# Optimization experiments

Hardware: AMD Instinct MI355X
Metric: run time of the kernel (lower is better)

## Reference

```python
import jax, jax.numpy as jnp
import numpy as np

NEG_INF = -4294967295.0  # -2**32 + 1, matches original padding value

def prelu(x, alpha):
    return jnp.where(x >= 0, x, alpha * x)

def setup_inputs() -> dict:
    key = jax.random.key(0)
    ks = jax.random.split(key, 12)
    B, T, D = 2048, 200, 64
    H0, H1 = 80, 40
    q = jax.random.normal(ks[0], (B, D), dtype=jnp.float32)
    k = jax.random.normal(ks[1], (B, T, D), dtype=jnp.float32)
    v = jax.random.normal(ks[2], (B, T, D), dtype=jnp.float32)
    mask = jax.random.randint(ks[3], (B, T), 0, 2, dtype=jnp.int32)
    Fin = 4 * D  # concat of q, k, q-k, q*k
    W0 = jax.random.normal(ks[4], (Fin, H0), dtype=jnp.float32) / np.sqrt(Fin)
    b0 = jnp.zeros((H0,), dtype=jnp.float32)
    a0 = jax.random.uniform(ks[5], (H0,), dtype=jnp.float32) * 0.25  # PReLU per-feature alpha
    W1 = jax.random.normal(ks[6], (H0, H1), dtype=jnp.float32) / np.sqrt(H0)
    b1 = jnp.zeros((H1,), dtype=jnp.float32)
    a1 = jax.random.uniform(ks[7], (H1,), dtype=jnp.float32) * 0.25
    Wo = jax.random.normal(ks[8], (H1, 1), dtype=jnp.float32) / np.sqrt(H1)
    bo = jnp.zeros((1,), dtype=jnp.float32)
    return {"q": q, "k": k, "v": v, "W0": W0, "b0": b0, "a0": a0,
            "W1": W1, "b1": b1, "a1": a1, "Wo": Wo, "bo": bo, "mask": mask}

def reference(q, k, v, W0, b0, a0, W1, b1, a1, Wo, bo, mask):
    # q: [B,D] -> broadcast to [B,T,D] (tile+reshape in original)
    qe = jnp.broadcast_to(q[:, None, :], k.shape)
    info = jnp.concatenate([qe, k, qe - k, qe * k], axis=-1)  # [B,T,4D]
    h = prelu(jnp.einsum('btf,fh->bth', info, W0) + b0, a0)    # [B,T,H0]
    h = prelu(jnp.einsum('bth,hg->btg', h, W1) + b1, a1)       # [B,T,H1]
    logits = (jnp.einsum('btg,go->bto', h, Wo) + bo)[..., 0]   # [B,T]
    logits = jnp.where(mask == 0, NEG_INF, logits)
    w = jax.nn.softmax(logits, axis=-1)                        # [B,T]
    out = jnp.einsum('bt,btd->bd', w, v)                       # [B,D]
    return out
```

## Files before the change

### kernel.cpp

```cpp
#include <hip/hip_runtime.h>
#include <hip/hip_bf16.h>
#include <math.h>

constexpr int D  = 64;
constexpr int T  = 200;
constexpr int H0 = 80;
constexpr int H1 = 40;
constexpr int BLOCK = 256;
constexpr float NEG_INF_V = -4294967295.0f;

typedef short short8 __attribute__((ext_vector_type(8)));
typedef float f32x4 __attribute__((ext_vector_type(4)));
typedef int   int4v __attribute__((ext_vector_type(4)));

__device__ inline unsigned short bf16h(float x) {
    __hip_bfloat16 t = __float2bfloat16(x);
    union { __hip_bfloat16 v; unsigned short u; } c; c.v = t; return c.u;
}
__device__ inline unsigned pk_bf16(float a, float b) {
    float2 f2; f2.x = a; f2.y = b;
    __hip_bfloat162 t = __float22bfloat162_rn(f2);
    union { __hip_bfloat162 v; unsigned u; } c; c.v = t; return c.u;
}
__device__ inline void pk_split(float a, float b, unsigned& hi, unsigned& lo) {
    hi = pk_bf16(a, b);
    const float e0 = a - __uint_as_float(hi << 16);
    const float e1 = b - __uint_as_float(hi & 0xffff0000u);
    lo = pk_bf16(e0, e1);
}
__device__ inline short8 mk8(int w0, int w1, int w2, int w3) {
    union { int4v i; short8 s; } u;
    u.i = (int4v){w0, w1, w2, w3};
    return u.s;
}
#define BPERM(ad, v) __builtin_amdgcn_ds_bpermute((ad), (int)(v))
#define MFMA(A, B, C) __builtin_amdgcn_mfma_f32_16x16x32_bf16((A), (B), (C), 0, 0, 0)

__global__ __launch_bounds__(BLOCK, 2) void attn_fused(
    const float* __restrict__ q, const float* __restrict__ k,
    const float* __restrict__ v, const float* __restrict__ W0,
    const float* __restrict__ b0, const float* __restrict__ a0,
    const float* __restrict__ W1, const float* __restrict__ b1,
    const float* __restrict__ a1, const float* __restrict__ Wo,
    const int* __restrict__ mask, float* __restrict__ out)
{
    __shared__ unsigned short s_wfHi[5120];
    __shared__ unsigned short s_wfLo[5120];
    __shared__ unsigned short s_w1Hi[4608];
    __shared__ unsigned short s_w1Lo[4608];
    __shared__ float s_logits[208];
    __shared__ float s_biasq[H0];
    __shared__ float s_a0[H0];
    __shared__ float s_b1p[48], s_a1p[48], s_Wop[48];
    __shared__ float s_w[BLOCK];
    __shared__ float s_red[8];
    __shared__ float s_part[4][D];

    const int tid  = threadIdx.x;
    const int b    = blockIdx.x;
    const int wv   = tid >> 6;
    const int lane = tid & 63;
    const int l16  = lane & 15;
    const int quad = lane >> 4;
    const bool hiQ = (quad >= 2);
    const float* qb = q + (size_t)b * D;

    const int mval = (tid < T) ? mask[(size_t)b * T + tid] : 0;
    float4 kc0, kc1, kc2, kc3;
    {
        int row = wv * 16 + l16; if (row > T - 1) row = T - 1;
        const float* kr = k + ((size_t)b * T + row) * D + quad * 8;
        kc0 = *(const float4*)(kr);
        kc1 = *(const float4*)(kr + 4);
        kc2 = *(const float4*)(kr + 32);
        kc3 = *(const float4*)(kr + 36);
    }

    const float* Wk = W0 + 64 * H0;
    const float* Wd = W0 + 128 * H0;
    const float* Wp = W0 + 192 * H0;
    #pragma unroll 4
    for (int it = 0; it < 20; ++it) {
        const int e  = it * 256 + tid;
        const int kk = e / 80, h = e - kk * 80;
        const float w = Wk[e] - Wd[e] + qb[kk] * Wp[e];
        const unsigned short hb = bf16h(w);
        const unsigned short lb = bf16h(w - __uint_as_float((unsigned)hb << 16));
        const int off = (((kk >> 5) * 5 + (h >> 4)) << 9)
                      + (((((kk >> 3) & 3) << 4) + (h & 15)) << 3) + (kk & 7);
        s_wfHi[off] = hb; s_wfLo[off] = lb;
    }
    #pragma unroll 4
    for (int it = 0; it < 18; ++it) {
        const int e  = it * 256 + tid;
        const int k2 = e / 48, n = e - k2 * 48;
        const float w = (k2 < H0 && n < H1) ? W1[k2 * H1 + n] : 0.0f;
        const unsigned short hb = bf16h(w);
        const unsigned short lb = bf16h(w - __uint_as_float((unsigned)hb << 16));
        const int off = (((k2 >> 5) * 3 + (n >> 4)) << 9)
                      + (((((k2 >> 3) & 3) << 4) + (n & 15)) << 3) + (k2 & 7);
        s_w1Hi[off] = hb; s_w1Lo[off] = lb;
    }
    if (tid < H0) {
        float acc = b0[tid];
        #pragma unroll 8
        for (int d = 0; d < D; ++d)
            acc = fmaf(qb[d], W0[d * H0 + tid] + W0[(128 + d) * H0 + tid], acc);
        s_biasq[tid] = acc;
        s_a0[tid]    = a0[tid];
    }
    if (tid < 48) {
        s_b1p[tid] = (tid < H1) ? b1[tid] : 0.0f;
        s_a1p[tid] = (tid < H1) ? a1[tid] : 0.0f;
        s_Wop[tid] = (tid < H1) ? Wo[tid] : 0.0f;
    }
    __syncthreads();

    const int addr0 = (((quad & 1) << 5) + l16) << 2;
    const int addr1 = addr0 + 64;

#define L1_HT(HT, HW, LW) { \
    f32x4 acc_ = {0.0f, 0.0f, 0.0f, 0.0f}; \
    { short8 Ah_ = *(const short8*)&s_wfHi[(0 * 5 + HT) * 512 + lane * 8]; \
      short8 Al_ = *(const short8*)&s_wfLo[(0 * 5 + HT) * 512 + lane * 8]; \
      acc_ = MFMA(Ah_, kbhi0, acc_); \
      acc_ = MFMA(Ah_, kblo0, acc_); \
      acc_ = MFMA(Al_, kbhi0, acc_); } \
    { short8 Ah_ = *(const short8*)&s_wfHi[(1 * 5 + HT) * 512 + lane * 8]; \
      short8 Al_ = *(const short8*)&s_wfLo[(1 * 5 + HT) * 512 + lane * 8]; \
      acc_ = MFMA(Ah_, kbhi1, acc_); \
      acc_ = MFMA(Ah_, kblo1, acc_); \
      acc_ = MFMA(Al_, kbhi1, acc_); } \
    const int hb_ = HT * 16 + quad * 4; \
    const float x0_ = acc_[0] + s_biasq[hb_ + 0]; \
    const float x1_ = acc_[1] + s_biasq[hb_ + 1]; \
    const float x2_ = acc_[2] + s_biasq[hb_ + 2]; \
    const float x3_ = acc_[3] + s_biasq[hb_ + 3]; \
    const float f0_ = (x0_ >= 0.0f) ? x0_ : s_a0[hb_ + 0] * x0_; \
    const float f1_ = (x1_ >= 0.0f) ? x1_ : s_a0[hb_ + 1] * x1_; \
    const float f2_ = (x2_ >= 0.0f) ? x2_ : s_a0[hb_ + 2] * x2_; \
    const float f3_ = (x3_ >= 0.0f) ? x3_ : s_a0[hb_ + 3] * x3_; \
    pk_split(f0_, f1_, HW.x, LW.x); \
    pk_split(f2_, f3_, HW.y, LW.y); }

#define TRN(HA, HB, LA, LB, AHI, ALO) { \
    int h0_ = BPERM(addr0, HA.x), h1_ = BPERM(addr0, HA.y); \
    int h2_ = BPERM(addr1, HA.x), h3_ = BPERM(addr1, HA.y); \
    int g0_ = BPERM(addr0, HB.x), g1_ = BPERM(addr0, HB.y); \
    int g2_ = BPERM(addr1, HB.x), g3_ = BPERM(addr1, HB.y); \
    AHI = mk8(hiQ ? g0_ : h0_, hiQ ? g1_ : h1_, hiQ ? g2_ : h2_, hiQ ? g3_ : h3_); \
    int l0_ = BPERM(addr0, LA.x), l1_ = BPERM(addr0, LA.y); \
    int l2_ = BPERM(addr1, LA.x), l3_ = BPERM(addr1, LA.y); \
    int m0_ = BPERM(addr0, LB.x), m1_ = BPERM(addr0, LB.y); \
    int m2_ = BPERM(addr1, LB.x), m3_ = BPERM(addr1, LB.y); \
    ALO = mk8(hiQ ? m0_ : l0_, hiQ ? m1_ : l1_, hiQ ? m2_ : l2_, hiQ ? m3_ : l3_); }

#define TRN2(HA, LA, AHI, ALO) { \
    int h0_ = BPERM(addr0, HA.x), h1_ = BPERM(addr0, HA.y); \
    int h2_ = BPERM(addr1, HA.x), h3_ = BPERM(addr1, HA.y); \
    AHI = mk8(hiQ ? 0 : h0_, hiQ ? 0 : h1_, hiQ ? 0 : h2_, hiQ ? 0 : h3_); \
    int l0_ = BPERM(addr0, LA.x), l1_ = BPERM(addr0, LA.y); \
    int l2_ = BPERM(addr1, LA.x), l3_ = BPERM(addr1, LA.y); \
    ALO = mk8(hiQ ? 0 : l0_, hiQ ? 0 : l1_, hiQ ? 0 : l2_, hiQ ? 0 : l3_); }

#define L2_NT(NT2) { \
    f32x4 acc_ = {0.0f, 0.0f, 0.0f, 0.0f}; \
    { short8 bh_ = *(const short8*)&s_w1Hi[(0 * 3 + NT2) * 512 + lane * 8]; \
      short8 bl_ = *(const short8*)&s_w1Lo[(0 * 3 + NT2) * 512 + lane * 8]; \
      acc_ = MFMA(a2hi0, bh_, acc_); \
      acc_ = MFMA(a2hi0, bl_, acc_); \
      acc_ = MFMA(a2lo0, bh_, acc_); } \
    { short8 bh_ = *(const short8*)&s_w1Hi[(1 * 3 + NT2) * 512 + lane * 8]; \
      short8 bl_ = *(const short8*)&s_w1Lo[(1 * 3 + NT2) * 512 + lane * 8]; \
      acc_ = MFMA(a2hi1, bh_, acc_); \
      acc_ = MFMA(a2hi1, bl_, acc_); \
      acc_ = MFMA(a2lo1, bh_, acc_); } \
    { short8 bh_ = *(const short8*)&s_w1Hi[(2 * 3 + NT2) * 512 + lane * 8]; \
      short8 bl_ = *(const short8*)&s_w1Lo[(2 * 3 + NT2) * 512 + lane * 8]; \
      acc_ = MFMA(a2hi2, bh_, acc_); \
      acc_ = MFMA(a2hi2, bl_, acc_); \
      acc_ = MFMA(a2lo2, bh_, acc_); } \
    const int g_ = NT2 * 16 + l16; \
    const float bg_ = s_b1p[g_], ag_ = s_a1p[g_], wg_ = s_Wop[g_]; \
    { const float x_ = acc_[0] + bg_; part0 = fmaf((x_ >= 0.0f) ? x_ : ag_ * x_, wg_, part0); } \
    { const float x_ = acc_[1] + bg_; part1 = fmaf((x_ >= 0.0f) ? x_ : ag_ * x_, wg_, part1); } \
    { const float x_ = acc_[2] + bg_; part2 = fmaf((x_ >= 0.0f) ? x_ : ag_ * x_, wg_, part2); } \
    { const float x_ = acc_[3] + bg_; part3 = fmaf((x_ >= 0.0f) ? x_ : ag_ * x_, wg_, part3); } }

    for (int mt = wv; mt < 13; mt += 4) {
        float4 kn0, kn1, kn2, kn3;
        const bool hasNext = (mt + 4 < 13);
        if (hasNext) {
            int row = (mt + 4) * 16 + l16; if (row > T - 1) row = T - 1;
            const float* kr = k + ((size_t)b * T + row) * D + quad * 8;
            kn0 = *(const float4*)(kr);
            kn1 = *(const float4*)(kr + 4);
            kn2 = *(const float4*)(kr + 32);
            kn3 = *(const float4*)(kr + 36);
        }
        short8 kbhi0, kblo0, kbhi1, kblo1;
        {
            unsigned h0_, l0_, h1_, l1_, h2_, l2_, h3_, l3_;
            pk_split(kc0.x, kc0.y, h0_, l0_);
            pk_split(kc0.z, kc0.w, h1_, l1_);
            pk_split(kc1.x, kc1.y, h2_, l2_);
            pk_split(kc1.z, kc1.w, h3_, l3_);
            kbhi0 = mk8((int)h0_, (int)h1_, (int)h2_, (int)h3_);
            kblo0 = mk8((int)l0_, (int)l1_, (int)l2_, (int)l3_);
            pk_split(kc2.x, kc2.y, h0_, l0_);
            pk_split(kc2.z, kc2.w, h1_, l1_);
            pk_split(kc3.x, kc3.y, h2_, l2_);
            pk_split(kc3.z, kc3.w, h3_, l3_);
            kbhi1 = mk8((int)h0_, (int)h1_, (int)h2_, (int)h3_);
            kblo1 = mk8((int)l0_, (int)l1_, (int)l2_, (int)l3_);
        }
        uint2 hw0, hw1, hw2, hw3, hw4, lw0, lw1, lw2, lw3, lw4;
        L1_HT(0, hw0, lw0)
        L1_HT(1, hw1, lw1)
        L1_HT(2, hw2, lw2)
        L1_HT(3, hw3, lw3)
        L1_HT(4, hw4, lw4)
        short8 a2hi0, a2lo0, a2hi1, a2lo1, a2hi2, a2lo2;
        TRN(hw0, hw1, lw0, lw1, a2hi0, a2lo0)
        TRN(hw2, hw3, lw2, lw3, a2hi1, a2lo1)
        TRN2(hw4, lw4, a2hi2, a2lo2)
        float part0 = 0.0f, part1 = 0.0f, part2 = 0.0f, part3 = 0.0f;
        L2_NT(0)
        L2_NT(1)
        L2_NT(2)
        #pragma unroll
        for (int off = 1; off < 16; off <<= 1) {
            part0 += __shfl_xor(part0, off);
            part1 += __shfl_xor(part1, off);
            part2 += __shfl_xor(part2, off);
            part3 += __shfl_xor(part3, off);
        }
        if (l16 == 0) {
            float4 p = {part0, part1, part2, part3};
            *(float4*)&s_logits[mt * 16 + quad * 4] = p;
        }
        if (hasNext) { kc0 = kn0; kc1 = kn1; kc2 = kn2; kc3 = kn3; }
    }
    __syncthreads();

    float logit = -INFINITY;
    if (tid < T)
        logit = (mval == 0) ? NEG_INF_V : s_logits[tid];

    float m = logit;
    #pragma unroll
    for (int off = 32; off > 0; off >>= 1) m = fmaxf(m, __shfl_xor(m, off));
    if (lane == 0) s_red[wv] = m;
    __syncthreads();
    m = fmaxf(fmaxf(s_red[0], s_red[1]), fmaxf(s_red[2], s_red[3]));
    const float e = expf(logit - m);
    s_w[tid] = e;
    float ssum = e;
    #pragma unroll
    for (int off = 32; off > 0; off >>= 1) ssum += __shfl_xor(ssum, off);
    if (lane == 0) s_red[4 + wv] = ssum;
    __syncthreads();
    const float inv = 1.0f / (s_red[4] + s_red[5] + s_red[6] + s_red[7]);

    const int d = tid & (D - 1);
    const int c = tid >> 6;
    constexpr int TC = T / 4;
    float acc2 = 0.0f;
    const float* vp = v + ((size_t)b * T + c * TC) * D + d;
    #pragma unroll 10
    for (int t = 0; t < TC; ++t)
        acc2 = fmaf(s_w[c * TC + t], vp[t * D], acc2);
    s_part[c][d] = acc2;
    __syncthreads();
    if (tid < D) {
        out[(size_t)b * D + tid] =
            (s_part[0][tid] + s_part[1][tid] + s_part[2][tid] + s_part[3][tid]) * inv;
    }
}

extern "C" void kernel_launch(void* const* d_in, const int* in_sizes, int n_in,
                              void* d_out, int out_size, void* d_ws, size_t ws_size,
                              hipStream_t stream) {
    const float* q  = (const float*)d_in[0];
    const float* k  = (const float*)d_in[1];
    const float* v  = (const float*)d_in[2];
    const float* W0 = (const float*)d_in[3];
    const float* b0 = (const float*)d_in[4];
    const float* a0 = (const float*)d_in[5];
    const float* W1 = (const float*)d_in[6];
    const float* b1 = (const float*)d_in[7];
    const float* a1 = (const float*)d_in[8];
    const float* Wo = (const float*)d_in[9];
    const int*  mask = (const int*)d_in[11];
    float* out = (float*)d_out;

    const int B = in_sizes[0] / D;

    attn_fused<<<dim3(B), dim3(BLOCK), 0, stream>>>(
        q, k, v, W0, b0, a0, W1, b1, a1, Wo, mask, out);
}
```

Baseline: 323.4 us.

## Process two row tiles per wave iteration with interleaved MFMA chains

Each wave now handles two 16-row k tiles at once (A and B), running their MFMA accumulation chains interleaved so independent MFMAs can hide each other's latency. Shared-memory weight fragments are loaded once and reused for both tiles, and the prefetch of k rows is doubled accordingly. The 13-tile loop becomes two iterations, with some tiles clamped to tile 12 and computed redundantly. The cost is higher register pressure and redundant work on the clamped tiles.

```diff
diff --git a/kernel.cpp b/kernel.cpp
--- a/kernel.cpp
+++ b/kernel.cpp
@@ -64,16 +64,19 @@
     const int quad = lane >> 4;
     const bool hiQ = (quad >= 2);
     const float* qb = q + (size_t)b * D;
+    const float* kb_base = k + (size_t)b * T * D;
 
     const int mval = (tid < T) ? mask[(size_t)b * T + tid] : 0;
-    float4 kc0, kc1, kc2, kc3;
+    float4 kA0, kA1, kA2, kA3, kB0, kB1, kB2, kB3;
     {
-        int row = wv * 16 + l16; if (row > T - 1) row = T - 1;
-        const float* kr = k + ((size_t)b * T + row) * D + quad * 8;
-        kc0 = *(const float4*)(kr);
-        kc1 = *(const float4*)(kr + 4);
-        kc2 = *(const float4*)(kr + 32);
-        kc3 = *(const float4*)(kr + 36);
+        int rA = wv * 16 + l16;        if (rA > T - 1) rA = T - 1;
+        int rB = (wv + 4) * 16 + l16;  if (rB > T - 1) rB = T - 1;
+        const float* pA = kb_base + (size_t)rA * D + quad * 8;
+        const float* pB = kb_base + (size_t)rB * D + quad * 8;
+        kA0 = *(const float4*)(pA);      kB0 = *(const float4*)(pB);
+        kA1 = *(const float4*)(pA + 4);  kB1 = *(const float4*)(pB + 4);
+        kA2 = *(const float4*)(pA + 32); kB2 = *(const float4*)(pB + 32);
+        kA3 = *(const float4*)(pA + 36); kB3 = *(const float4*)(pB + 36);
     }
 
     const float* Wk = W0 + 64 * H0;
@@ -119,29 +122,48 @@
     const int addr0 = (((quad & 1) << 5) + l16) << 2;
     const int addr1 = addr0 + 64;
 
-#define L1_HT(HT, HW, LW) { \
-    f32x4 acc_ = {0.0f, 0.0f, 0.0f, 0.0f}; \
-    { short8 Ah_ = *(const short8*)&s_wfHi[(0 * 5 + HT) * 512 + lane * 8]; \
-      short8 Al_ = *(const short8*)&s_wfLo[(0 * 5 + HT) * 512 + lane * 8]; \
-      acc_ = MFMA(Ah_, kbhi0, acc_); \
-      acc_ = MFMA(Ah_, kblo0, acc_); \
-      acc_ = MFMA(Al_, kbhi0, acc_); } \
-    { short8 Ah_ = *(const short8*)&s_wfHi[(1 * 5 + HT) * 512 + lane * 8]; \
-      short8 Al_ = *(const short8*)&s_wfLo[(1 * 5 + HT) * 512 + lane * 8]; \
-      acc_ = MFMA(Ah_, kbhi1, acc_); \
-      acc_ = MFMA(Ah_, kblo1, acc_); \
-      acc_ = MFMA(Al_, kbhi1, acc_); } \
+#define KBUILD(C0, C1, C2, C3, BH0, BL0, BH1, BL1) { \
+    unsigned h0_, l0_, h1_, l1_, h2_, l2_, h3_, l3_; \
+    pk_split(C0.x, C0.y, h0_, l0_); pk_split(C0.z, C0.w, h1_, l1_); \
+    pk_split(C1.x, C1.y, h2_, l2_); pk_split(C1.z, C1.w, h3_, l3_); \
+    BH0 = mk8((int)h0_, (int)h1_, (int)h2_, (int)h3_); \
+    BL0 = mk8((int)l0_, (int)l1_, (int)l2_, (int)l3_); \
+    pk_split(C2.x, C2.y, h0_, l0_); pk_split(C2.z, C2.w, h1_, l1_); \
+    pk_split(C3.x, C3.y, h2_, l2_); pk_split(C3.z, C3.w, h3_, l3_); \
+    BH1 = mk8((int)h0_, (int)h1_, (int)h2_, (int)h3_); \
+    BL1 = mk8((int)l0_, (int)l1_, (int)l2_, (int)l3_); }
+
+#define L1_NT(HT, HWA, LWA, HWB, LWB) { \
+    const short8 Ah0_ = *(const short8*)&s_wfHi[(0 * 5 + HT) * 512 + lane * 8]; \
+    const short8 Al0_ = *(const short8*)&s_wfLo[(0 * 5 + HT) * 512 + lane * 8]; \
+    const short8 Ah1_ = *(const short8*)&s_wfHi[(1 * 5 + HT) * 512 + lane * 8]; \
+    const short8 Al1_ = *(const short8*)&s_wfLo[(1 * 5 + HT) * 512 + lane * 8]; \
+    f32x4 aA_ = {0.0f, 0.0f, 0.0f, 0.0f}, aB_ = {0.0f, 0.0f, 0.0f, 0.0f}; \
+    aA_ = MFMA(Ah0_, kAhi0, aA_);  aB_ = MFMA(Ah0_, kBhi0, aB_); \
+    aA_ = MFMA(Ah0_, kAlo0, aA_);  aB_ = MFMA(Ah0_, kBlo0, aB_); \
+    aA_ = MFMA(Al0_, kAhi0, aA_);  aB_ = MFMA(Al0_, kBhi0, aB_); \
+    aA_ = MFMA(Ah1_, kAhi1, aA_);  aB_ = MFMA(Ah1_, kBhi1, aB_); \
+    aA_ = MFMA(Ah1_, kAlo1, aA_);  aB_ = MFMA(Ah1_, kBlo1, aB_); \
+    aA_ = MFMA(Al1_, kAhi1, aA_);  aB_ = MFMA(Al1_, kBhi1, aB_); \
     const int hb_ = HT * 16 + quad * 4; \
-    const float x0_ = acc_[0] + s_biasq[hb_ + 0]; \
-    const float x1_ = acc_[1] + s_biasq[hb_ + 1]; \
-    const float x2_ = acc_[2] + s_biasq[hb_ + 2]; \
-    const float x3_ = acc_[3] + s_biasq[hb_ + 3]; \
-    const float f0_ = (x0_ >= 0.0f) ? x0_ : s_a0[hb_ + 0] * x0_; \
-    const float f1_ = (x1_ >= 0.0f) ? x1_ : s_a0[hb_ + 1] * x1_; \
-    const float f2_ = (x2_ >= 0.0f) ? x2_ : s_a0[hb_ + 2] * x2_; \
-    const float f3_ = (x3_ >= 0.0f) ? x3_ : s_a0[hb_ + 3] * x3_; \
-    pk_split(f0_, f1_, HW.x, LW.x); \
-    pk_split(f2_, f3_, HW.y, LW.y); }
+    const float c0_ = s_biasq[hb_ + 0], c1_ = s_biasq[hb_ + 1]; \
+    const float c2_ = s_biasq[hb_ + 2], c3_ = s_biasq[hb_ + 3]; \
+    const float p0_ = s_a0[hb_ + 0], p1_ = s_a0[hb_ + 1]; \
+    const float p2_ = s_a0[hb_ + 2], p3_ = s_a0[hb_ + 3]; \
+    { const float x0_ = aA_[0] + c0_, x1_ = aA_[1] + c1_; \
+      const float x2_ = aA_[2] + c2_, x3_ = aA_[3] + c3_; \
+      const float f0_ = (x0_ >= 0.0f) ? x0_ : p0_ * x0_; \
+      const float f1_ = (x1_ >= 0.0f) ? x1_ : p1_ * x1_; \
+      const float f2_ = (x2_ >= 0.0f) ? x2_ : p2_ * x2_; \
+      const float f3_ = (x3_ >= 0.0f) ? x3_ : p3_ * x3_; \
+      pk_split(f0_, f1_, HWA.x, LWA.x); pk_split(f2_, f3_, HWA.y, LWA.y); } \
+    { const float x0_ = aB_[0] + c0_, x1_ = aB_[1] + c1_; \
+      const float x2_ = aB_[2] + c2_, x3_ = aB_[3] + c3_; \
+      const float f0_ = (x0_ >= 0.0f) ? x0_ : p0_ * x0_; \
+      const float f1_ = (x1_ >= 0.0f) ? x1_ : p1_ * x1_; \
+      const float f2_ = (x2_ >= 0.0f) ? x2_ : p2_ * x2_; \
+      const float f3_ = (x3_ >= 0.0f) ? x3_ : p3_ * x3_; \
+      pk_split(f0_, f1_, HWB.x, LWB.x); pk_split(f2_, f3_, HWB.y, LWB.y); } }
 
 #define TRN(HA, HB, LA, LB, AHI, ALO) { \
     int h0_ = BPERM(addr0, HA.x), h1_ = BPERM(addr0, HA.y); \
@@ -164,82 +186,92 @@
     ALO = mk8(hiQ ? 0 : l0_, hiQ ? 0 : l1_, hiQ ? 0 : l2_, hiQ ? 0 : l3_); }
 
 #define L2_NT(NT2) { \
-    f32x4 acc_ = {0.0f, 0.0f, 0.0f, 0.0f}; \
-    { short8 bh_ = *(const short8*)&s_w1Hi[(0 * 3 + NT2) * 512 + lane * 8]; \
-      short8 bl_ = *(const short8*)&s_w1Lo[(0 * 3 + NT2) * 512 + lane * 8]; \
-      acc_ = MFMA(a2hi0, bh_, acc_); \
-      acc_ = MFMA(a2hi0, bl_, acc_); \
-      acc_ = MFMA(a2lo0, bh_, acc_); } \
-    { short8 bh_ = *(const short8*)&s_w1Hi[(1 * 3 + NT2) * 512 + lane * 8]; \
-      short8 bl_ = *(const short8*)&s_w1Lo[(1 * 3 + NT2) * 512 + lane * 8]; \
-      acc_ = MFMA(a2hi1, bh_, acc_); \
-      acc_ = MFMA(a2hi1, bl_, acc_); \
-      acc_ = MFMA(a2lo1, bh_, acc_); } \
-    { short8 bh_ = *(const short8*)&s_w1Hi[(2 * 3 + NT2) * 512 + lane * 8]; \
-      short8 bl_ = *(const short8*)&s_w1Lo[(2 * 3 + NT2) * 512 + lane * 8]; \
-      acc_ = MFMA(a2hi2, bh_, acc_); \
-      acc_ = MFMA(a2hi2, bl_, acc_); \
-      acc_ = MFMA(a2lo2, bh_, acc_); } \
+    f32x4 aA_ = {0.0f, 0.0f, 0.0f, 0.0f}, aB_ = {0.0f, 0.0f, 0.0f, 0.0f}; \
+    { const short8 bh_ = *(const short8*)&s_w1Hi[(0 * 3 + NT2) * 512 + lane * 8]; \
+      const short8 bl_ = *(const short8*)&s_w1Lo[(0 * 3 + NT2) * 512 + lane * 8]; \
+      aA_ = MFMA(a2Ahi0, bh_, aA_);  aB_ = MFMA(a2Bhi0, bh_, aB_); \
+      aA_ = MFMA(a2Ahi0, bl_, aA_);  aB_ = MFMA(a2Bhi0, bl_, aB_); \
+      aA_ = MFMA(a2Alo0, bh_, aA_);  aB_ = MFMA(a2Blo0, bh_, aB_); } \
+    { const short8 bh_ = *(const short8*)&s_w1Hi[(1 * 3 + NT2) * 512 + lane * 8]; \
+      const short8 bl_ = *(const short8*)&s_w1Lo[(1 * 3 + NT2) * 512 + lane * 8]; \
+      aA_ = MFMA(a2Ahi1, bh_, aA_);  aB_ = MFMA(a2Bhi1, bh_, aB_); \
+      aA_ = MFMA(a2Ahi1, bl_, aA_);  aB_ = MFMA(a2Bhi1, bl_, aB_); \
+      aA_ = MFMA(a2Alo1, bh_, aA_);  aB_ = MFMA(a2Blo1, bh_, aB_); } \
+    { const short8 bh_ = *(const short8*)&s_w1Hi[(2 * 3 + NT2) * 512 + lane * 8]; \
+      const short8 bl_ = *(const short8*)&s_w1Lo[(2 * 3 + NT2) * 512 + lane * 8]; \
+      aA_ = MFMA(a2Ahi2, bh_, aA_);  aB_ = MFMA(a2Bhi2, bh_, aB_); \
+      aA_ = MFMA(a2Ahi2, bl_, aA_);  aB_ = MFMA(a2Bhi2, bl_, aB_); \
+      aA_ = MFMA(a2Alo2, bh_, aA_);  aB_ = MFMA(a2Blo2, bh_, aB_); } \
     const int g_ = NT2 * 16 + l16; \
     const float bg_ = s_b1p[g_], ag_ = s_a1p[g_], wg_ = s_Wop[g_]; \
-    { const float x_ = acc_[0] + bg_; part0 = fmaf((x_ >= 0.0f) ? x_ : ag_ * x_, wg_, part0); } \
-    { const float x_ = acc_[1] + bg_; part1 = fmaf((x_ >= 0.0f) ? x_ : ag_ * x_, wg_, part1); } \
-    { const float x_ = acc_[2] + bg_; part2 = fmaf((x_ >= 0.0f) ? x_ : ag_ * x_, wg_, part2); } \
-    { const float x_ = acc_[3] + bg_; part3 = fmaf((x_ >= 0.0f) ? x_ : ag_ * x_, wg_, part3); } }
-
-    for (int mt = wv; mt < 13; mt += 4) {
-        float4 kn0, kn1, kn2, kn3;
-        const bool hasNext = (mt + 4 < 13);
-        if (hasNext) {
-            int row = (mt + 4) * 16 + l16; if (row > T - 1) row = T - 1;
-            const float* kr = k + ((size_t)b * T + row) * D + quad * 8;
-            kn0 = *(const float4*)(kr);
-            kn1 = *(const float4*)(kr + 4);
-            kn2 = *(const float4*)(kr + 32);
-            kn3 = *(const float4*)(kr + 36);
+    { const float x_ = aA_[0] + bg_; partA0 = fmaf((x_ >= 0.0f) ? x_ : ag_ * x_, wg_, partA0); } \
+    { const float x_ = aA_[1] + bg_; partA1 = fmaf((x_ >= 0.0f) ? x_ : ag_ * x_, wg_, partA1); } \
+    { const float x_ = aA_[2] + bg_; partA2 = fmaf((x_ >= 0.0f) ? x_ : ag_ * x_, wg_, partA2); } \
+    { const float x_ = aA_[3] + bg_; partA3 = fmaf((x_ >= 0.0f) ? x_ : ag_ * x_, wg_, partA3); } \
+    { const float x_ = aB_[0] + bg_; partB0 = fmaf((x_ >= 0.0f) ? x_ : ag_ * x_, wg_, partB0); } \
+    { const float x_ = aB_[1] + bg_; partB1 = fmaf((x_ >= 0.0f) ? x_ : ag_ * x_, wg_, partB1); } \
+    { const float x_ = aB_[2] + bg_; partB2 = fmaf((x_ >= 0.0f) ? x_ : ag_ * x_, wg_, partB2); } \
+    { const float x_ = aB_[3] + bg_; partB3 = fmaf((x_ >= 0.0f) ? x_ : ag_ * x_, wg_, partB3); } }
+
+    for (int ii = 0; ii < 2; ++ii) {
+        const int mtA = wv + ii * 8;
+        const int mtB = (mtA + 4 > 12) ? 12 : (mtA + 4);
+        float4 nA0, nA1, nA2, nA3, nB0, nB1, nB2, nB3;
+        if (ii == 0) {
+            int rA = (wv + 8) * 16 + l16;                 if (rA > T - 1) rA = T - 1;
+            int tB = (wv + 12 > 12) ? 12 : (wv + 12);
+            int rB = tB * 16 + l16;                       if (rB > T - 1) rB = T - 1;
+            const float* pA = kb_base + (size_t)rA * D + quad * 8;
+            const float* pB = kb_base + (size_t)rB * D + quad * 8;
+            nA0 = *(const float4*)(pA);      nB0 = *(const float4*)(pB);
+            nA1 = *(const float4*)(pA + 4);  nB1 = *(const float4*)(pB + 4);
+            nA2 = *(const float4*)(pA + 32); nB2 = *(const float4*)(pB + 32);
+            nA3 = *(const float4*)(pA + 36); nB3 = *(const float4*)(pB + 36);
         }
-        short8 kbhi0, kblo0, kbhi1, kblo1;
-        {
-            unsigned h0_, l0_, h1_, l1_, h2_, l2_, h3_, l3_;
-            pk_split(kc0.x, kc0.y, h0_, l0_);
-            pk_split(kc0.z, kc0.w, h1_, l1_);
-            pk_split(kc1.x, kc1.y, h2_, l2_);
-            pk_split(kc1.z, kc1.w, h3_, l3_);
-            kbhi0 = mk8((int)h0_, (int)h1_, (int)h2_, (int)h3_);
-            kblo0 = mk8((int)l0_, (int)l1_, (int)l2_, (int)l3_);
-            pk_split(kc2.x, kc2.y, h0_, l0_);
-            pk_split(kc2.z, kc2.w, h1_, l1_);
-            pk_split(kc3.x, kc3.y, h2_, l2_);
-            pk_split(kc3.z, kc3.w, h3_, l3_);
-            kbhi1 = mk8((int)h0_, (int)h1_, (int)h2_, (int)h3_);
-            kblo1 = mk8((int)l0_, (int)l1_, (int)l2_, (int)l3_);
-        }
-        uint2 hw0, hw1, hw2, hw3, hw4, lw0, lw1, lw2, lw3, lw4;
-        L1_HT(0, hw0, lw0)
-        L1_HT(1, hw1, lw1)
-        L1_HT(2, hw2, lw2)
-        L1_HT(3, hw3, lw3)
-        L1_HT(4, hw4, lw4)
-        short8 a2hi0, a2lo0, a2hi1, a2lo1, a2hi2, a2lo2;
-        TRN(hw0, hw1, lw0, lw1, a2hi0, a2lo0)
-        TRN(hw2, hw3, lw2, lw3, a2hi1, a2lo1)
-        TRN2(hw4, lw4, a2hi2, a2lo2)
-        float part0 = 0.0f, part1 = 0.0f, part2 = 0.0f, part3 = 0.0f;
+        short8 kAhi0, kAlo0, kAhi1, kAlo1, kBhi0, kBlo0, kBhi1, kBlo1;
+        KBUILD(kA0, kA1, kA2, kA3, kAhi0, kAlo0, kAhi1, kAlo1)
+        KBUILD(kB0, kB1, kB2, kB3, kBhi0, kBlo0, kBhi1, kBlo1)
+        uint2 hwA0, hwA1, hwA2, hwA3, hwA4, lwA0, lwA1, lwA2, lwA3, lwA4;
+        uint2 hwB0, hwB1, hwB2, hwB3, hwB4, lwB0, lwB1, lwB2, lwB3, lwB4;
+        L1_NT(0, hwA0, lwA0, hwB0, lwB0)
+        L1_NT(1, hwA1, lwA1, hwB1, lwB1)
+        L1_NT(2, hwA2, lwA2, hwB2, lwB2)
+        L1_NT(3, hwA3, lwA3, hwB3, lwB3)
+        L1_NT(4, hwA4, lwA4, hwB4, lwB4)
+        short8 a2Ahi0, a2Alo0, a2Ahi1, a2Alo1, a2Ahi2, a2Alo2;
+        short8 a2Bhi0, a2Blo0, a2Bhi1, a2Blo1, a2Bhi2, a2Blo2;
+        TRN(hwA0, hwA1, lwA0, lwA1, a2Ahi0, a2Alo0)
+        TRN(hwA2, hwA3, lwA2, lwA3, a2Ahi1, a2Alo1)
+        TRN2(hwA4, lwA4, a2Ahi2, a2Alo2)
+        TRN(hwB0, hwB1, lwB0, lwB1, a2Bhi0, a2Blo0)
+        TRN(hwB2, hwB3, lwB2, lwB3, a2Bhi1, a2Blo1)
+        TRN2(hwB4, lwB4, a2Bhi2, a2Blo2)
+        float partA0 = 0.0f, partA1 = 0.0f, partA2 = 0.0f, partA3 = 0.0f;
+        float partB0 = 0.0f, partB1 = 0.0f, partB2 = 0.0f, partB3 = 0.0f;
         L2_NT(0)
         L2_NT(1)
         L2_NT(2)
         #pragma unroll
         for (int off = 1; off < 16; off <<= 1) {
-            part0 += __shfl_xor(part0, off);
-            part1 += __shfl_xor(part1, off);
-            part2 += __shfl_xor(part2, off);
-            part3 += __shfl_xor(part3, off);
+            partA0 += __shfl_xor(partA0, off);
+            partA1 += __shfl_xor(partA1, off);
+            partA2 += __shfl_xor(partA2, off);
+            partA3 += __shfl_xor(partA3, off);
+            partB0 += __shfl_xor(partB0, off);
+            partB1 += __shfl_xor(partB1, off);
+            partB2 += __shfl_xor(partB2, off);
+            partB3 += __shfl_xor(partB3, off);
         }
         if (l16 == 0) {
-            float4 p = {part0, part1, part2, part3};
-            *(float4*)&s_logits[mt * 16 + quad * 4] = p;
+            float4 pA = {partA0, partA1, partA2, partA3};
+            float4 pB = {partB0, partB1, partB2, partB3};
+            *(float4*)&s_logits[mtA * 16 + quad * 4] = pA;
+            *(float4*)&s_logits[mtB * 16 + quad * 4] = pB;
         }
-        if (hasNext) { kc0 = kn0; kc1 = kn1; kc2 = kn2; kc3 = kn3; }
+        if (ii == 0) {
+            kA0 = nA0; kA1 = nA1; kA2 = nA2; kA3 = nA3;
+            kB0 = nB0; kB1 = nB1; kB2 = nB2; kB3 = nB3;
+        }
     }
     __syncthreads();
 
```

Result: slower. 369.9 us (+14.4%).

## Pre-split W1 into bf16 hi/lo in a prep kernel and read from global

Applied to the files above, without the earlier changes.

Moves the per-block W1 bf16 hi/lo split and swizzle into a separate one-block kernel that writes into workspace. The main kernel then reads the MFMA B operands straight from global/L2 instead of LDS, which frees about 18 KB of shared memory and removes per-block prologue work. The k prefetch is also restructured to overwrite the current registers right after they are converted, which saves the extra register set. The trade-offs are an extra kernel launch and global loads inside the inner MFMA loop in place of LDS reads.

```diff
diff --git a/kernel.cpp b/kernel.cpp
--- a/kernel.cpp
+++ b/kernel.cpp
@@ -36,18 +36,33 @@
 #define BPERM(ad, v) __builtin_amdgcn_ds_bpermute((ad), (int)(v))
 #define MFMA(A, B, C) __builtin_amdgcn_mfma_f32_16x16x32_bf16((A), (B), (C), 0, 0, 0)
 
+__global__ __launch_bounds__(256) void fold_w1(
+    const float* __restrict__ W1, short* __restrict__ w1fHi,
+    short* __restrict__ w1fLo)
+{
+    const int tid = threadIdx.x;
+    for (int e = tid; e < 4608; e += 256) {
+        const int k2 = e / 48, n = e - k2 * 48;
+        const float w = (k2 < H0 && n < H1) ? W1[k2 * H1 + n] : 0.0f;
+        const unsigned short hb = bf16h(w);
+        const unsigned short lb = bf16h(w - __uint_as_float((unsigned)hb << 16));
+        const int off = (((k2 >> 5) * 3 + (n >> 4)) << 9)
+                      + (((((k2 >> 3) & 3) << 4) + (n & 15)) << 3) + (k2 & 7);
+        w1fHi[off] = hb; w1fLo[off] = lb;
+    }
+}
+
 __global__ __launch_bounds__(BLOCK, 2) void attn_fused(
     const float* __restrict__ q, const float* __restrict__ k,
     const float* __restrict__ v, const float* __restrict__ W0,
     const float* __restrict__ b0, const float* __restrict__ a0,
-    const float* __restrict__ W1, const float* __restrict__ b1,
-    const float* __restrict__ a1, const float* __restrict__ Wo,
-    const int* __restrict__ mask, float* __restrict__ out)
+    const short* __restrict__ w1fHi, const short* __restrict__ w1fLo,
+    const float* __restrict__ b1, const float* __restrict__ a1,
+    const float* __restrict__ Wo, const int* __restrict__ mask,
+    float* __restrict__ out)
 {
     __shared__ unsigned short s_wfHi[5120];
     __shared__ unsigned short s_wfLo[5120];
-    __shared__ unsigned short s_w1Hi[4608];
-    __shared__ unsigned short s_w1Lo[4608];
     __shared__ float s_logits[208];
     __shared__ float s_biasq[H0];
     __shared__ float s_a0[H0];
@@ -64,12 +79,13 @@
     const int quad = lane >> 4;
     const bool hiQ = (quad >= 2);
     const float* qb = q + (size_t)b * D;
+    const float* kb_base = k + (size_t)b * T * D;
 
     const int mval = (tid < T) ? mask[(size_t)b * T + tid] : 0;
     float4 kc0, kc1, kc2, kc3;
     {
         int row = wv * 16 + l16; if (row > T - 1) row = T - 1;
-        const float* kr = k + ((size_t)b * T + row) * D + quad * 8;
+        const float* kr = kb_base + (size_t)row * D + quad * 8;
         kc0 = *(const float4*)(kr);
         kc1 = *(const float4*)(kr + 4);
         kc2 = *(const float4*)(kr + 32);
@@ -89,17 +105,6 @@
         const int off = (((kk >> 5) * 5 + (h >> 4)) << 9)
                       + (((((kk >> 3) & 3) << 4) + (h & 15)) << 3) + (kk & 7);
         s_wfHi[off] = hb; s_wfLo[off] = lb;
-    }
-    #pragma unroll 4
-    for (int it = 0; it < 18; ++it) {
-        const int e  = it * 256 + tid;
-        const int k2 = e / 48, n = e - k2 * 48;
-        const float w = (k2 < H0 && n < H1) ? W1[k2 * H1 + n] : 0.0f;
-        const unsigned short hb = bf16h(w);
-        const unsigned short lb = bf16h(w - __uint_as_float((unsigned)hb << 16));
-        const int off = (((k2 >> 5) * 3 + (n >> 4)) << 9)
-                      + (((((k2 >> 3) & 3) << 4) + (n & 15)) << 3) + (k2 & 7);
-        s_w1Hi[off] = hb; s_w1Lo[off] = lb;
     }
     if (tid < H0) {
         float acc = b0[tid];
@@ -165,18 +170,18 @@
 
 #define L2_NT(NT2) { \
     f32x4 acc_ = {0.0f, 0.0f, 0.0f, 0.0f}; \
-    { short8 bh_ = *(const short8*)&s_w1Hi[(0 * 3 + NT2) * 512 + lane * 8]; \
-      short8 bl_ = *(const short8*)&s_w1Lo[(0 * 3 + NT2) * 512 + lane * 8]; \
+    { short8 bh_ = *(const short8*)&w1fHi[(0 * 3 + NT2) * 512 + lane * 8]; \
+      short8 bl_ = *(const short8*)&w1fLo[(0 * 3 + NT2) * 512 + lane * 8]; \
       acc_ = MFMA(a2hi0, bh_, acc_); \
       acc_ = MFMA(a2hi0, bl_, acc_); \
       acc_ = MFMA(a2lo0, bh_, acc_); } \
-    { short8 bh_ = *(const short8*)&s_w1Hi[(1 * 3 + NT2) * 512 + lane * 8]; \
-      short8 bl_ = *(const short8*)&s_w1Lo[(1 * 3 + NT2) * 512 + lane * 8]; \
+    { short8 bh_ = *(const short8*)&w1fHi[(1 * 3 + NT2) * 512 + lane * 8]; \
+      short8 bl_ = *(const short8*)&w1fLo[(1 * 3 + NT2) * 512 + lane * 8]; \
       acc_ = MFMA(a2hi1, bh_, acc_); \
       acc_ = MFMA(a2hi1, bl_, acc_); \
       acc_ = MFMA(a2lo1, bh_, acc_); } \
-    { short8 bh_ = *(const short8*)&s_w1Hi[(2 * 3 + NT2) * 512 + lane * 8]; \
-      short8 bl_ = *(const short8*)&s_w1Lo[(2 * 3 + NT2) * 512 + lane * 8]; \
+    { short8 bh_ = *(const short8*)&w1fHi[(2 * 3 + NT2) * 512 + lane * 8]; \
+      short8 bl_ = *(const short8*)&w1fLo[(2 * 3 + NT2) * 512 + lane * 8]; \
       acc_ = MFMA(a2hi2, bh_, acc_); \
       acc_ = MFMA(a2hi2, bl_, acc_); \
       acc_ = MFMA(a2lo2, bh_, acc_); } \
@@ -188,16 +193,6 @@
     { const float x_ = acc_[3] + bg_; part3 = fmaf((x_ >= 0.0f) ? x_ : ag_ * x_, wg_, part3); } }
 
     for (int mt = wv; mt < 13; mt += 4) {
-        float4 kn0, kn1, kn2, kn3;
-        const bool hasNext = (mt + 4 < 13);
-        if (hasNext) {
-            int row = (mt + 4) * 16 + l16; if (row > T - 1) row = T - 1;
-            const float* kr = k + ((size_t)b * T + row) * D + quad * 8;
-            kn0 = *(const float4*)(kr);
-            kn1 = *(const float4*)(kr + 4);
-            kn2 = *(const float4*)(kr + 32);
-            kn3 = *(const float4*)(kr + 36);
-        }
         short8 kbhi0, kblo0, kbhi1, kblo1;
         {
             unsigned h0_, l0_, h1_, l1_, h2_, l2_, h3_, l3_;
@@ -213,6 +208,14 @@
             pk_split(kc3.z, kc3.w, h3_, l3_);
             kbhi1 = mk8((int)h0_, (int)h1_, (int)h2_, (int)h3_);
             kblo1 = mk8((int)l0_, (int)l1_, (int)l2_, (int)l3_);
+        }
+        if (mt + 4 < 13) {
+            int row = (mt + 4) * 16 + l16; if (row > T - 1) row = T - 1;
+            const float* kr = kb_base + (size_t)row * D + quad * 8;
+            kc0 = *(const float4*)(kr);
+            kc1 = *(const float4*)(kr + 4);
+            kc2 = *(const float4*)(kr + 32);
+            kc3 = *(const float4*)(kr + 36);
         }
         uint2 hw0, hw1, hw2, hw3, hw4, lw0, lw1, lw2, lw3, lw4;
         L1_HT(0, hw0, lw0)
@@ -239,7 +242,6 @@
             float4 p = {part0, part1, part2, part3};
             *(float4*)&s_logits[mt * 16 + quad * 4] = p;
         }
-        if (hasNext) { kc0 = kn0; kc1 = kn1; kc2 = kn2; kc3 = kn3; }
     }
     __syncthreads();
 
@@ -296,6 +298,10 @@
 
     const int B = in_sizes[0] / D;
 
+    short* w1fHi = (short*)d_ws;
+    short* w1fLo = w1fHi + 4608;
+
+    fold_w1<<<dim3(1), dim3(256), 0, stream>>>(W1, w1fHi, w1fLo);
     attn_fused<<<dim3(B), dim3(BLOCK), 0, stream>>>(
-        q, k, v, W0, b0, a0, W1, b1, a1, Wo, mask, out);
-}
+        q, k, v, W0, b0, a0, w1fHi, w1fLo, b1, a1, Wo, mask, out);
+}
```

Result: faster. 303.6 us (-6.1%).
